# Kernel optimization log

Measured on AMD Instinct MI355X. Metric: run time of the kernel, lower is better.

The kernel has to match this reference:

```python
import jax, jax.numpy as jnp
import numpy as np

EPS = 1e-6

def setup_inputs() -> dict:
    key = jax.random.key(0)
    kq, kk, kv = jax.random.split(key, 3)
    B, H, S, D = 4, 16, 2048, 64
    q = jax.random.normal(kq, (B, H, S, D), dtype=jnp.float32)
    k = jax.random.normal(kk, (B, H, S, D), dtype=jnp.float32)
    v = jax.random.normal(kv, (B, H, S, D), dtype=jnp.float32)
    return {"q": q, "k": k, "v": v}

def reference(q, k, v):
    # ReBASED parallel attention: squared QK^T scores, causal mask, sum-normalized.
    scale = q.shape[-1] ** (-0.5)
    q = q * scale
    # attn: [B, H, S, S]
    attn = jnp.einsum('bhqd,bhkd->bhqk', q, k)
    attn = attn * attn  # squared scores
    S = q.shape[-2]
    causal = jnp.tril(jnp.ones((S, S), dtype=bool))
    attn = jnp.where(causal, attn, 0.0)
    o = jnp.einsum('bhqk,bhkd->bhqd', attn, v)
    z = attn.sum(-1, keepdims=True)
    return o / (z + EPS)
```

## Files before the change

kernel.cpp:

```cpp
#include <hip/hip_runtime.h>
#include <hip/hip_bf16.h>


#define SEQ 2048
#define HD  64
#define BQ  128
#define BK  64
#define LQ  72
#define LV  76

typedef __attribute__((ext_vector_type(8))) short bf16x8;
typedef __attribute__((ext_vector_type(4))) short bf16x4;
typedef __attribute__((ext_vector_type(4))) float f32x4;

__device__ inline unsigned packbf(float a, float b) {
    __hip_bfloat162 h = __float22bfloat162_rn(make_float2(a, b));
    union { __hip_bfloat162 h2; unsigned u; } cv; cv.h2 = h; return cv.u;
}

__global__ __launch_bounds__(256, 2)
void rebased_r3_kernel(const float* __restrict__ qg,
                       const float* __restrict__ kg,
                       const float* __restrict__ vg,
                       float* __restrict__ og) {
    __shared__ __align__(16) unsigned short Qs[BQ][LQ];
    __shared__ __align__(16) unsigned short Ks[2][BK][LQ];
    __shared__ __align__(16) unsigned short Vst[2][HD][LV];

    const int t    = threadIdx.x;
    const int lane = t & 63;
    const int w    = t >> 6;
    const int li   = lane & 15;
    const int qd   = lane >> 4;
    const int pj   = blockIdx.x;
    const int head = blockIdx.y;
    const size_t base = (size_t)head * SEQ * HD;

    #pragma unroll
    for (int seg = 0; seg < 2; ++seg) {
        const int qt = seg ? pj : (15 - pj);
        const int ktmax = 2 * qt + 1;

        float4 qreg[8], kreg[4], vreg[4];
        {
            const float4* qsrc = (const float4*)(qg + base + (size_t)qt * BQ * HD);
            #pragma unroll
            for (int l = 0; l < 8; ++l) qreg[l] = qsrc[t + l * 256];
            const float4* ksrc = (const float4*)(kg + base);
            const float4* vsrc = (const float4*)(vg + base);
            #pragma unroll
            for (int l = 0; l < 4; ++l) kreg[l] = ksrc[t + l * 256];
            const int d4g = t & 15, rp = t >> 4;
            #pragma unroll
            for (int p = 0; p < 2; ++p) {
                int r0 = p * 32 + rp * 2;
                vreg[2 * p]     = vsrc[r0 * 16 + d4g];
                vreg[2 * p + 1] = vsrc[(r0 + 1) * 16 + d4g];
            }
        }
        __syncthreads();

        #pragma unroll
        for (int l = 0; l < 8; ++l) {
            int f = t + l * 256, row = f >> 4, d4 = (f & 15) << 2;
            unsigned* dst = (unsigned*)&Qs[row][d4];
            dst[0] = packbf(qreg[l].x * 0.125f, qreg[l].y * 0.125f);
            dst[1] = packbf(qreg[l].z * 0.125f, qreg[l].w * 0.125f);
        }
        #pragma unroll
        for (int l = 0; l < 4; ++l) {
            int row = (t >> 4) + l * 16, d4 = (t & 15) << 2;
            unsigned* dst = (unsigned*)&Ks[0][row][d4];
            dst[0] = packbf(kreg[l].x, kreg[l].y);
            dst[1] = packbf(kreg[l].z, kreg[l].w);
        }
        {
            const int d4g = t & 15, rp = t >> 4;
            #pragma unroll
            for (int p = 0; p < 2; ++p) {
                int r0 = p * 32 + rp * 2;
                float a0[4] = {vreg[2*p].x, vreg[2*p].y, vreg[2*p].z, vreg[2*p].w};
                float a1[4] = {vreg[2*p+1].x, vreg[2*p+1].y, vreg[2*p+1].z, vreg[2*p+1].w};
                #pragma unroll
                for (int j = 0; j < 4; ++j)
                    *(unsigned*)&Vst[0][d4g * 4 + j][r0] = packbf(a0[j], a1[j]);
            }
        }
        __syncthreads();

        f32x4 oacc[2][4];
        float zpart[2] = {0.f, 0.f};
        #pragma unroll
        for (int mt = 0; mt < 2; ++mt)
            #pragma unroll
            for (int nd = 0; nd < 4; ++nd) oacc[mt][nd] = (f32x4){0.f, 0.f, 0.f, 0.f};

        for (int kt = 0; kt <= ktmax; ++kt) {
            const int cur = kt & 1;

            if (kt < ktmax) {
                const float4* ksrc = (const float4*)(kg + base + (size_t)(kt + 1) * BK * HD);
                const float4* vsrc = (const float4*)(vg + base + (size_t)(kt + 1) * BK * HD);
                #pragma unroll
                for (int l = 0; l < 4; ++l) kreg[l] = ksrc[t + l * 256];
                const int d4g = t & 15, rp = t >> 4;
                #pragma unroll
                for (int p = 0; p < 2; ++p) {
                    int r0 = p * 32 + rp * 2;
                    vreg[2 * p]     = vsrc[r0 * 16 + d4g];
                    vreg[2 * p + 1] = vsrc[(r0 + 1) * 16 + d4g];
                }
            }

            const int qrow_min = qt * BQ + w * 32;
            const bool active   = (kt * BK <= qrow_min + 31);
            const bool needmask = (kt * BK + 63 > qrow_min);

            if (active) {
                f32x4 stt[4][2];
                #pragma unroll
                for (int nk = 0; nk < 4; ++nk)
                    #pragma unroll
                    for (int mt = 0; mt < 2; ++mt) stt[nk][mt] = (f32x4){0.f,0.f,0.f,0.f};
                #pragma unroll
                for (int ks = 0; ks < 2; ++ks) {
                    const int kb = ks * 32 + qd * 8;
                    bf16x8 kf[4], qf[2];
                    #pragma unroll
                    for (int nk = 0; nk < 4; ++nk)
                        kf[nk] = *(const bf16x8*)&Ks[cur][nk * 16 + li][kb];
                    #pragma unroll
                    for (int mt = 0; mt < 2; ++mt)
                        qf[mt] = *(const bf16x8*)&Qs[w * 32 + mt * 16 + li][kb];
                    #pragma unroll
                    for (int nk = 0; nk < 4; ++nk)
                        #pragma unroll
                        for (int mt = 0; mt < 2; ++mt)
                            stt[nk][mt] = __builtin_amdgcn_mfma_f32_16x16x32_bf16(
                                kf[nk], qf[mt], stt[nk][mt], 0, 0, 0);
                }

                unsigned pk[4][2][2];
                #pragma unroll
                for (int nk = 0; nk < 4; ++nk) {
                    const int kcb = kt * BK + nk * 16 + qd * 4;
                    #pragma unroll
                    for (int mt = 0; mt < 2; ++mt) {
                        const int qrow = qrow_min + mt * 16 + li;
                        float p[4];
                        #pragma unroll
                        for (int r = 0; r < 4; ++r) {
                            float s = stt[nk][mt][r];
                            if (needmask && (kcb + r > qrow)) s = 0.f;
                            p[r] = s * s;
                        }
                        zpart[mt] += (p[0] + p[1]) + (p[2] + p[3]);
                        pk[nk][mt][0] = packbf(p[0], p[1]);
                        pk[nk][mt][1] = packbf(p[2], p[3]);
                    }
                }

                #pragma unroll
                for (int ks16 = 0; ks16 < 4; ++ks16) {
                    bf16x4 av[2];
                    #pragma unroll
                    for (int mt = 0; mt < 2; ++mt) {
                        union { unsigned u[2]; bf16x4 v; } cv;
                        cv.u[0] = pk[ks16][mt][0]; cv.u[1] = pk[ks16][mt][1];
                        av[mt] = cv.v;
                    }
                    #pragma unroll
                    for (int nd = 0; nd < 4; ++nd) {
                        bf16x4 vf = *(const bf16x4*)&Vst[cur][nd * 16 + li][ks16 * 16 + qd * 4];
                        #pragma unroll
                        for (int mt = 0; mt < 2; ++mt)
                            oacc[mt][nd] = __builtin_amdgcn_mfma_f32_16x16x16bf16_1k(
                                av[mt], vf, oacc[mt][nd], 0, 0, 0);
                    }
                }
            }

            if (kt < ktmax) {
                const int nb = cur ^ 1;
                #pragma unroll
                for (int l = 0; l < 4; ++l) {
                    int row = (t >> 4) + l * 16, d4 = (t & 15) << 2;
                    unsigned* dst = (unsigned*)&Ks[nb][row][d4];
                    dst[0] = packbf(kreg[l].x, kreg[l].y);
                    dst[1] = packbf(kreg[l].z, kreg[l].w);
                }
                const int d4g = t & 15, rp = t >> 4;
                #pragma unroll
                for (int p = 0; p < 2; ++p) {
                    int r0 = p * 32 + rp * 2;
                    float a0[4] = {vreg[2*p].x, vreg[2*p].y, vreg[2*p].z, vreg[2*p].w};
                    float a1[4] = {vreg[2*p+1].x, vreg[2*p+1].y, vreg[2*p+1].z, vreg[2*p+1].w};
                    #pragma unroll
                    for (int j = 0; j < 4; ++j)
                        *(unsigned*)&Vst[nb][d4g * 4 + j][r0] = packbf(a0[j], a1[j]);
                }
            }
            __syncthreads();
        }

        float* odst = og + base + (size_t)qt * BQ * HD;
        #pragma unroll
        for (int mt = 0; mt < 2; ++mt) {
            float zf = zpart[mt];
            zf += __shfl_xor(zf, 16, 64);
            zf += __shfl_xor(zf, 32, 64);
            #pragma unroll
            for (int r = 0; r < 4; ++r) {
                float zr = __shfl(zf, qd * 4 + r, 64);
                float inv = 1.f / (zr + 1e-6f);
                int row = w * 32 + mt * 16 + qd * 4 + r;
                #pragma unroll
                for (int nd = 0; nd < 4; ++nd)
                    odst[row * HD + nd * 16 + li] = oacc[mt][nd][r] * inv;
            }
        }
    }
}

extern "C" void kernel_launch(void* const* d_in, const int* in_sizes, int n_in,
                              void* d_out, int out_size, void* d_ws, size_t ws_size,
                              hipStream_t stream) {
    const float* q = (const float*)d_in[0];
    const float* k = (const float*)d_in[1];
    const float* v = (const float*)d_in[2];
    float* out = (float*)d_out;

    dim3 grid(8, 64);
    dim3 block(256);
    rebased_r3_kernel<<<grid, block, 0, stream>>>(q, k, v, out);
}
```

Before: 209.3 us.

## Switch to 32x32x16 MFMA with Q fragments held in registers

Replaces the 16x16 MFMA tiles with 32x32x16 bf16 MFMA for both the QK^T and PV products. Each wave now loads its own Q rows straight from global memory into register fragments, so the shared Q tile and its LDS reads go away. The squared-score fragments are rearranged across half-waves with a shuffle to form the PV operand, and V is now stored in a padded row layout. This is meant to cut LDS traffic and MFMA instruction count. In exchange it adds cross-lane shuffles, a larger accumulator register footprint, and a transposed output store pattern.

```diff
diff --git a/kernel.cpp b/kernel.cpp
--- a/kernel.cpp
+++ b/kernel.cpp
@@ -6,51 +6,63 @@
 #define HD  64
 #define BQ  128
 #define BK  64
-#define LQ  72
-#define LV  76
-
-typedef __attribute__((ext_vector_type(8))) short bf16x8;
-typedef __attribute__((ext_vector_type(4))) short bf16x4;
-typedef __attribute__((ext_vector_type(4))) float f32x4;
+#define LK  72
+
+typedef __attribute__((ext_vector_type(8)))  short bf16x8;
+typedef __attribute__((ext_vector_type(16))) float f32x16;
 
 __device__ inline unsigned packbf(float a, float b) {
-    __hip_bfloat162 h = __float22bfloat162_rn(make_float2(a, b));
-    union { __hip_bfloat162 h2; unsigned u; } cv; cv.h2 = h; return cv.u;
+    __hip_bfloat162 hh = __float22bfloat162_rn(make_float2(a, b));
+    union { __hip_bfloat162 h2; unsigned u; } cv; cv.h2 = hh; return cv.u;
 }
 
 __global__ __launch_bounds__(256, 2)
-void rebased_r3_kernel(const float* __restrict__ qg,
+void rebased_r4_kernel(const float* __restrict__ qg,
                        const float* __restrict__ kg,
                        const float* __restrict__ vg,
                        float* __restrict__ og) {
-    __shared__ __align__(16) unsigned short Qs[BQ][LQ];
-    __shared__ __align__(16) unsigned short Ks[2][BK][LQ];
-    __shared__ __align__(16) unsigned short Vst[2][HD][LV];
+    __shared__ __align__(16) unsigned short Ks[2][BK][LK];
+    __shared__ __align__(16) unsigned short Vs[2][HD][LK];
 
     const int t    = threadIdx.x;
     const int lane = t & 63;
     const int w    = t >> 6;
-    const int li   = lane & 15;
-    const int qd   = lane >> 4;
+    const int l5   = lane & 31;
+    const int h    = lane >> 5;
     const int pj   = blockIdx.x;
     const int head = blockIdx.y;
     const size_t base = (size_t)head * SEQ * HD;
+    const int d4g = t & 15, rp = t >> 4;
 
     #pragma unroll
     for (int seg = 0; seg < 2; ++seg) {
         const int qt = seg ? pj : (15 - pj);
         const int ktmax = 2 * qt + 1;
-
-        float4 qreg[8], kreg[4], vreg[4];
+        const int qrow_min = qt * BQ + w * 32;
+        const int qrow = qrow_min + l5;
+
+        bf16x8 qf[4];
         {
-            const float4* qsrc = (const float4*)(qg + base + (size_t)qt * BQ * HD);
-            #pragma unroll
-            for (int l = 0; l < 8; ++l) qreg[l] = qsrc[t + l * 256];
+            const float* qp = qg + base + (size_t)qrow * HD + 8 * h;
+            #pragma unroll
+            for (int ds = 0; ds < 4; ++ds) {
+                float4 a = *(const float4*)(qp + ds * 16);
+                float4 b = *(const float4*)(qp + ds * 16 + 4);
+                union { unsigned u[4]; bf16x8 v; } cv;
+                cv.u[0] = packbf(a.x * 0.125f, a.y * 0.125f);
+                cv.u[1] = packbf(a.z * 0.125f, a.w * 0.125f);
+                cv.u[2] = packbf(b.x * 0.125f, b.y * 0.125f);
+                cv.u[3] = packbf(b.z * 0.125f, b.w * 0.125f);
+                qf[ds] = cv.v;
+            }
+        }
+
+        float4 kreg[4], vreg[4];
+        {
             const float4* ksrc = (const float4*)(kg + base);
             const float4* vsrc = (const float4*)(vg + base);
             #pragma unroll
             for (int l = 0; l < 4; ++l) kreg[l] = ksrc[t + l * 256];
-            const int d4g = t & 15, rp = t >> 4;
             #pragma unroll
             for (int p = 0; p < 2; ++p) {
                 int r0 = p * 32 + rp * 2;
@@ -61,39 +73,27 @@
         __syncthreads();
 
         #pragma unroll
-        for (int l = 0; l < 8; ++l) {
+        for (int l = 0; l < 4; ++l) {
             int f = t + l * 256, row = f >> 4, d4 = (f & 15) << 2;
-            unsigned* dst = (unsigned*)&Qs[row][d4];
-            dst[0] = packbf(qreg[l].x * 0.125f, qreg[l].y * 0.125f);
-            dst[1] = packbf(qreg[l].z * 0.125f, qreg[l].w * 0.125f);
-        }
-        #pragma unroll
-        for (int l = 0; l < 4; ++l) {
-            int row = (t >> 4) + l * 16, d4 = (t & 15) << 2;
             unsigned* dst = (unsigned*)&Ks[0][row][d4];
             dst[0] = packbf(kreg[l].x, kreg[l].y);
             dst[1] = packbf(kreg[l].z, kreg[l].w);
         }
-        {
-            const int d4g = t & 15, rp = t >> 4;
-            #pragma unroll
-            for (int p = 0; p < 2; ++p) {
-                int r0 = p * 32 + rp * 2;
-                float a0[4] = {vreg[2*p].x, vreg[2*p].y, vreg[2*p].z, vreg[2*p].w};
-                float a1[4] = {vreg[2*p+1].x, vreg[2*p+1].y, vreg[2*p+1].z, vreg[2*p+1].w};
-                #pragma unroll
-                for (int j = 0; j < 4; ++j)
-                    *(unsigned*)&Vst[0][d4g * 4 + j][r0] = packbf(a0[j], a1[j]);
-            }
+        #pragma unroll
+        for (int p = 0; p < 2; ++p) {
+            int r0 = p * 32 + rp * 2;
+            float a0[4] = {vreg[2*p].x, vreg[2*p].y, vreg[2*p].z, vreg[2*p].w};
+            float a1[4] = {vreg[2*p+1].x, vreg[2*p+1].y, vreg[2*p+1].z, vreg[2*p+1].w};
+            #pragma unroll
+            for (int j = 0; j < 4; ++j)
+                *(unsigned*)&Vs[0][d4g * 4 + j][r0] = packbf(a0[j], a1[j]);
         }
         __syncthreads();
 
-        f32x4 oacc[2][4];
-        float zpart[2] = {0.f, 0.f};
-        #pragma unroll
-        for (int mt = 0; mt < 2; ++mt)
-            #pragma unroll
-            for (int nd = 0; nd < 4; ++nd) oacc[mt][nd] = (f32x4){0.f, 0.f, 0.f, 0.f};
+        f32x16 oa0, oa1;
+        #pragma unroll
+        for (int i = 0; i < 16; ++i) { oa0[i] = 0.f; oa1[i] = 0.f; }
+        float zadd = 0.f;
 
         for (int kt = 0; kt <= ktmax; ++kt) {
             const int cur = kt & 1;
@@ -103,7 +103,6 @@
                 const float4* vsrc = (const float4*)(vg + base + (size_t)(kt + 1) * BK * HD);
                 #pragma unroll
                 for (int l = 0; l < 4; ++l) kreg[l] = ksrc[t + l * 256];
-                const int d4g = t & 15, rp = t >> 4;
                 #pragma unroll
                 for (int p = 0; p < 2; ++p) {
                     int r0 = p * 32 + rp * 2;
@@ -112,71 +111,56 @@
                 }
             }
 
-            const int qrow_min = qt * BQ + w * 32;
-            const bool active   = (kt * BK <= qrow_min + 31);
-            const bool needmask = (kt * BK + 63 > qrow_min);
-
-            if (active) {
-                f32x4 stt[4][2];
-                #pragma unroll
-                for (int nk = 0; nk < 4; ++nk)
+            if (kt * 64 <= qrow_min + 31) {
+                f32x16 st0, st1;
+                #pragma unroll
+                for (int i = 0; i < 16; ++i) { st0[i] = 0.f; st1[i] = 0.f; }
+                #pragma unroll
+                for (int ds = 0; ds < 4; ++ds) {
+                    bf16x8 k0 = *(const bf16x8*)&Ks[cur][l5][ds * 16 + 8 * h];
+                    bf16x8 k1 = *(const bf16x8*)&Ks[cur][32 + l5][ds * 16 + 8 * h];
+                    st0 = __builtin_amdgcn_mfma_f32_32x32x16_bf16(k0, qf[ds], st0, 0, 0, 0);
+                    st1 = __builtin_amdgcn_mfma_f32_32x32x16_bf16(k1, qf[ds], st1, 0, 0, 0);
+                }
+
+                unsigned ppk[2][4][2];
+                const bool needmask = (kt * 64 + 63 > qrow_min);
+                const int kbase = kt * 64 + 4 * h;
+                #pragma unroll
+                for (int Mt = 0; Mt < 2; ++Mt) {
                     #pragma unroll
-                    for (int mt = 0; mt < 2; ++mt) stt[nk][mt] = (f32x4){0.f,0.f,0.f,0.f};
-                #pragma unroll
-                for (int ks = 0; ks < 2; ++ks) {
-                    const int kb = ks * 32 + qd * 8;
-                    bf16x8 kf[4], qf[2];
-                    #pragma unroll
-                    for (int nk = 0; nk < 4; ++nk)
-                        kf[nk] = *(const bf16x8*)&Ks[cur][nk * 16 + li][kb];
-                    #pragma unroll
-                    for (int mt = 0; mt < 2; ++mt)
-                        qf[mt] = *(const bf16x8*)&Qs[w * 32 + mt * 16 + li][kb];
-                    #pragma unroll
-                    for (int nk = 0; nk < 4; ++nk)
-                        #pragma unroll
-                        for (int mt = 0; mt < 2; ++mt)
-                            stt[nk][mt] = __builtin_amdgcn_mfma_f32_16x16x32_bf16(
-                                kf[nk], qf[mt], stt[nk][mt], 0, 0, 0);
-                }
-
-                unsigned pk[4][2][2];
-                #pragma unroll
-                for (int nk = 0; nk < 4; ++nk) {
-                    const int kcb = kt * BK + nk * 16 + qd * 4;
-                    #pragma unroll
-                    for (int mt = 0; mt < 2; ++mt) {
-                        const int qrow = qrow_min + mt * 16 + li;
+                    for (int r2 = 0; r2 < 4; ++r2) {
                         float p[4];
                         #pragma unroll
-                        for (int r = 0; r < 4; ++r) {
-                            float s = stt[nk][mt][r];
-                            if (needmask && (kcb + r > qrow)) s = 0.f;
-                            p[r] = s * s;
+                        for (int e = 0; e < 4; ++e) {
+                            float s = Mt ? st1[4 * r2 + e] : st0[4 * r2 + e];
+                            float pv = s * s;
+                            if (needmask && (kbase + 32 * Mt + 8 * r2 + e > qrow)) pv = 0.f;
+                            p[e] = pv;
                         }
-                        zpart[mt] += (p[0] + p[1]) + (p[2] + p[3]);
-                        pk[nk][mt][0] = packbf(p[0], p[1]);
-                        pk[nk][mt][1] = packbf(p[2], p[3]);
+                        zadd += (p[0] + p[1]) + (p[2] + p[3]);
+                        ppk[Mt][r2][0] = packbf(p[0], p[1]);
+                        ppk[Mt][r2][1] = packbf(p[2], p[3]);
                     }
                 }
 
                 #pragma unroll
-                for (int ks16 = 0; ks16 < 4; ++ks16) {
-                    bf16x4 av[2];
-                    #pragma unroll
-                    for (int mt = 0; mt < 2; ++mt) {
-                        union { unsigned u[2]; bf16x4 v; } cv;
-                        cv.u[0] = pk[ks16][mt][0]; cv.u[1] = pk[ks16][mt][1];
-                        av[mt] = cv.v;
-                    }
-                    #pragma unroll
-                    for (int nd = 0; nd < 4; ++nd) {
-                        bf16x4 vf = *(const bf16x4*)&Vst[cur][nd * 16 + li][ks16 * 16 + qd * 4];
-                        #pragma unroll
-                        for (int mt = 0; mt < 2; ++mt)
-                            oacc[mt][nd] = __builtin_amdgcn_mfma_f32_16x16x16bf16_1k(
-                                av[mt], vf, oacc[mt][nd], 0, 0, 0);
-                    }
+                for (int kst = 0; kst < 4; ++kst) {
+                    const int b0 = 2 * kst, b1 = 2 * kst + 1;
+                    unsigned a0 = ppk[b0 >> 2][b0 & 3][0], a1 = ppk[b0 >> 2][b0 & 3][1];
+                    unsigned c0 = ppk[b1 >> 2][b1 & 3][0], c1 = ppk[b1 >> 2][b1 & 3][1];
+                    unsigned s0 = h ? a0 : c0, s1 = h ? a1 : c1;
+                    unsigned g0 = (unsigned)__shfl_xor((int)s0, 32, 64);
+                    unsigned g1 = (unsigned)__shfl_xor((int)s1, 32, 64);
+                    union { unsigned u[4]; bf16x8 v; } pa;
+                    pa.u[0] = h ? g0 : a0;
+                    pa.u[1] = h ? g1 : a1;
+                    pa.u[2] = h ? c0 : g0;
+                    pa.u[3] = h ? c1 : g1;
+                    bf16x8 v0 = *(const bf16x8*)&Vs[cur][l5][kst * 16 + 8 * h];
+                    bf16x8 v1 = *(const bf16x8*)&Vs[cur][32 + l5][kst * 16 + 8 * h];
+                    oa0 = __builtin_amdgcn_mfma_f32_32x32x16_bf16(pa.v, v0, oa0, 0, 0, 0);
+                    oa1 = __builtin_amdgcn_mfma_f32_32x32x16_bf16(pa.v, v1, oa1, 0, 0, 0);
                 }
             }
 
@@ -184,12 +168,11 @@
                 const int nb = cur ^ 1;
                 #pragma unroll
                 for (int l = 0; l < 4; ++l) {
-                    int row = (t >> 4) + l * 16, d4 = (t & 15) << 2;
+                    int f = t + l * 256, row = f >> 4, d4 = (f & 15) << 2;
                     unsigned* dst = (unsigned*)&Ks[nb][row][d4];
                     dst[0] = packbf(kreg[l].x, kreg[l].y);
                     dst[1] = packbf(kreg[l].z, kreg[l].w);
                 }
-                const int d4g = t & 15, rp = t >> 4;
                 #pragma unroll
                 for (int p = 0; p < 2; ++p) {
                     int r0 = p * 32 + rp * 2;
@@ -197,27 +180,22 @@
                     float a1[4] = {vreg[2*p+1].x, vreg[2*p+1].y, vreg[2*p+1].z, vreg[2*p+1].w};
                     #pragma unroll
                     for (int j = 0; j < 4; ++j)
-                        *(unsigned*)&Vst[nb][d4g * 4 + j][r0] = packbf(a0[j], a1[j]);
+                        *(unsigned*)&Vs[nb][d4g * 4 + j][r0] = packbf(a0[j], a1[j]);
                 }
             }
             __syncthreads();
         }
 
-        float* odst = og + base + (size_t)qt * BQ * HD;
-        #pragma unroll
-        for (int mt = 0; mt < 2; ++mt) {
-            float zf = zpart[mt];
-            zf += __shfl_xor(zf, 16, 64);
-            zf += __shfl_xor(zf, 32, 64);
-            #pragma unroll
-            for (int r = 0; r < 4; ++r) {
-                float zr = __shfl(zf, qd * 4 + r, 64);
-                float inv = 1.f / (zr + 1e-6f);
-                int row = w * 32 + mt * 16 + qd * 4 + r;
-                #pragma unroll
-                for (int nd = 0; nd < 4; ++nd)
-                    odst[row * HD + nd * 16 + li] = oacc[mt][nd][r] * inv;
-            }
+        float zf = zadd + __shfl_xor(zadd, 32, 64);
+        float zinv = 1.f / (zf + 1e-6f);
+        float* odst = og + base + (size_t)(qt * BQ) * HD;
+        #pragma unroll
+        for (int r = 0; r < 16; ++r) {
+            int rowi = (r & 3) + 8 * (r >> 2) + 4 * h;
+            float inv = __shfl(zinv, rowi, 64);
+            int rg = w * 32 + rowi;
+            odst[(size_t)rg * HD + l5]      = oa0[r] * inv;
+            odst[(size_t)rg * HD + 32 + l5] = oa1[r] * inv;
         }
     }
 }
@@ -232,5 +210,5 @@
 
     dim3 grid(8, 64);
     dim3 block(256);
-    rebased_r3_kernel<<<grid, block, 0, stream>>>(q, k, v, out);
+    rebased_r4_kernel<<<grid, block, 0, stream>>>(q, k, v, out);
 }
```

Result: no change. 211.2 us (+0.9%).

## Shrink query tile to 64 rows with register-resident Q and remapped 1D grid

Applied to the files above, without the earlier changes.

Cuts the query tile from 128 to 64 rows, so each wave handles 16 query rows. Q fragments are loaded straight from global memory into registers, and the Q shared-memory buffer is removed. The grid becomes 1D with 1024 blocks in a head-interleaved order, and launch bounds are raised to 4 blocks per SM. This targets higher occupancy and finer causal load balance. In exchange, K/V tiles are loaded and converted twice as often per query row, and the wave-level skip of inactive key tiles is dropped.

```diff
diff --git a/kernel.cpp b/kernel.cpp
--- a/kernel.cpp
+++ b/kernel.cpp
@@ -4,9 +4,8 @@
 
 #define SEQ 2048
 #define HD  64
-#define BQ  128
 #define BK  64
-#define LQ  72
+#define LK  72
 #define LV  76
 
 typedef __attribute__((ext_vector_type(8))) short bf16x8;
@@ -14,17 +13,16 @@
 typedef __attribute__((ext_vector_type(4))) float f32x4;
 
 __device__ inline unsigned packbf(float a, float b) {
-    __hip_bfloat162 h = __float22bfloat162_rn(make_float2(a, b));
-    union { __hip_bfloat162 h2; unsigned u; } cv; cv.h2 = h; return cv.u;
+    __hip_bfloat162 hh = __float22bfloat162_rn(make_float2(a, b));
+    union { __hip_bfloat162 h2; unsigned u; } cv; cv.h2 = hh; return cv.u;
 }
 
-__global__ __launch_bounds__(256, 2)
-void rebased_r3_kernel(const float* __restrict__ qg,
+__global__ __launch_bounds__(256, 4)
+void rebased_r5_kernel(const float* __restrict__ qg,
                        const float* __restrict__ kg,
                        const float* __restrict__ vg,
                        float* __restrict__ og) {
-    __shared__ __align__(16) unsigned short Qs[BQ][LQ];
-    __shared__ __align__(16) unsigned short Ks[2][BK][LQ];
+    __shared__ __align__(16) unsigned short Ks[2][BK][LK];
     __shared__ __align__(16) unsigned short Vst[2][HD][LV];
 
     const int t    = threadIdx.x;
@@ -32,25 +30,42 @@
     const int w    = t >> 6;
     const int li   = lane & 15;
     const int qd   = lane >> 4;
-    const int pj   = blockIdx.x;
-    const int head = blockIdx.y;
+    const int id   = blockIdx.x;
+    const int xm   = id & 7;
+    const int qq   = id >> 3;
+    const int pj   = qq & 15;
+    const int head = xm + 8 * (qq >> 4);
     const size_t base = (size_t)head * SEQ * HD;
+    const int d4g = t & 15, rp = t >> 4;
 
     #pragma unroll
     for (int seg = 0; seg < 2; ++seg) {
-        const int qt = seg ? pj : (15 - pj);
-        const int ktmax = 2 * qt + 1;
-
-        float4 qreg[8], kreg[4], vreg[4];
+        const int qt = seg ? pj : (31 - pj);
+        const int ktmax = qt;
+        const int qrow = qt * 64 + w * 16 + li;
+
+        bf16x8 qf[2];
         {
-            const float4* qsrc = (const float4*)(qg + base + (size_t)qt * BQ * HD);
-            #pragma unroll
-            for (int l = 0; l < 8; ++l) qreg[l] = qsrc[t + l * 256];
+            const float* qp = qg + base + (size_t)qrow * HD + qd * 8;
+            #pragma unroll
+            for (int ks = 0; ks < 2; ++ks) {
+                float4 a = *(const float4*)(qp + ks * 32);
+                float4 b = *(const float4*)(qp + ks * 32 + 4);
+                union { unsigned u[4]; bf16x8 v; } cv;
+                cv.u[0] = packbf(a.x * 0.125f, a.y * 0.125f);
+                cv.u[1] = packbf(a.z * 0.125f, a.w * 0.125f);
+                cv.u[2] = packbf(b.x * 0.125f, b.y * 0.125f);
+                cv.u[3] = packbf(b.z * 0.125f, b.w * 0.125f);
+                qf[ks] = cv.v;
+            }
+        }
+
+        float4 kreg[4], vreg[4];
+        {
             const float4* ksrc = (const float4*)(kg + base);
             const float4* vsrc = (const float4*)(vg + base);
             #pragma unroll
             for (int l = 0; l < 4; ++l) kreg[l] = ksrc[t + l * 256];
-            const int d4g = t & 15, rp = t >> 4;
             #pragma unroll
             for (int p = 0; p < 2; ++p) {
                 int r0 = p * 32 + rp * 2;
@@ -61,39 +76,27 @@
         __syncthreads();
 
         #pragma unroll
-        for (int l = 0; l < 8; ++l) {
+        for (int l = 0; l < 4; ++l) {
             int f = t + l * 256, row = f >> 4, d4 = (f & 15) << 2;
-            unsigned* dst = (unsigned*)&Qs[row][d4];
-            dst[0] = packbf(qreg[l].x * 0.125f, qreg[l].y * 0.125f);
-            dst[1] = packbf(qreg[l].z * 0.125f, qreg[l].w * 0.125f);
-        }
-        #pragma unroll
-        for (int l = 0; l < 4; ++l) {
-            int row = (t >> 4) + l * 16, d4 = (t & 15) << 2;
             unsigned* dst = (unsigned*)&Ks[0][row][d4];
             dst[0] = packbf(kreg[l].x, kreg[l].y);
             dst[1] = packbf(kreg[l].z, kreg[l].w);
         }
-        {
-            const int d4g = t & 15, rp = t >> 4;
-            #pragma unroll
-            for (int p = 0; p < 2; ++p) {
-                int r0 = p * 32 + rp * 2;
-                float a0[4] = {vreg[2*p].x, vreg[2*p].y, vreg[2*p].z, vreg[2*p].w};
-                float a1[4] = {vreg[2*p+1].x, vreg[2*p+1].y, vreg[2*p+1].z, vreg[2*p+1].w};
-                #pragma unroll
-                for (int j = 0; j < 4; ++j)
-                    *(unsigned*)&Vst[0][d4g * 4 + j][r0] = packbf(a0[j], a1[j]);
-            }
+        #pragma unroll
+        for (int p = 0; p < 2; ++p) {
+            int r0 = p * 32 + rp * 2;
+            float a0[4] = {vreg[2*p].x, vreg[2*p].y, vreg[2*p].z, vreg[2*p].w};
+            float a1[4] = {vreg[2*p+1].x, vreg[2*p+1].y, vreg[2*p+1].z, vreg[2*p+1].w};
+            #pragma unroll
+            for (int j = 0; j < 4; ++j)
+                *(unsigned*)&Vst[0][d4g * 4 + j][r0] = packbf(a0[j], a1[j]);
         }
         __syncthreads();
 
-        f32x4 oacc[2][4];
-        float zpart[2] = {0.f, 0.f};
-        #pragma unroll
-        for (int mt = 0; mt < 2; ++mt)
-            #pragma unroll
-            for (int nd = 0; nd < 4; ++nd) oacc[mt][nd] = (f32x4){0.f, 0.f, 0.f, 0.f};
+        f32x4 oacc[4];
+        #pragma unroll
+        for (int nd = 0; nd < 4; ++nd) oacc[nd] = (f32x4){0.f, 0.f, 0.f, 0.f};
+        float zpart = 0.f;
 
         for (int kt = 0; kt <= ktmax; ++kt) {
             const int cur = kt & 1;
@@ -103,7 +106,6 @@
                 const float4* vsrc = (const float4*)(vg + base + (size_t)(kt + 1) * BK * HD);
                 #pragma unroll
                 for (int l = 0; l < 4; ++l) kreg[l] = ksrc[t + l * 256];
-                const int d4g = t & 15, rp = t >> 4;
                 #pragma unroll
                 for (int p = 0; p < 2; ++p) {
                     int r0 = p * 32 + rp * 2;
@@ -112,71 +114,49 @@
                 }
             }
 
-            const int qrow_min = qt * BQ + w * 32;
-            const bool active   = (kt * BK <= qrow_min + 31);
-            const bool needmask = (kt * BK + 63 > qrow_min);
-
-            if (active) {
-                f32x4 stt[4][2];
+            f32x4 stt[4];
+            #pragma unroll
+            for (int nk = 0; nk < 4; ++nk) stt[nk] = (f32x4){0.f, 0.f, 0.f, 0.f};
+            #pragma unroll
+            for (int ks = 0; ks < 2; ++ks) {
+                const int kb = ks * 32 + qd * 8;
+                bf16x8 kf[4];
                 #pragma unroll
                 for (int nk = 0; nk < 4; ++nk)
-                    #pragma unroll
-                    for (int mt = 0; mt < 2; ++mt) stt[nk][mt] = (f32x4){0.f,0.f,0.f,0.f};
-                #pragma unroll
-                for (int ks = 0; ks < 2; ++ks) {
-                    const int kb = ks * 32 + qd * 8;
-                    bf16x8 kf[4], qf[2];
-                    #pragma unroll
-                    for (int nk = 0; nk < 4; ++nk)
-                        kf[nk] = *(const bf16x8*)&Ks[cur][nk * 16 + li][kb];
-                    #pragma unroll
-                    for (int mt = 0; mt < 2; ++mt)
-                        qf[mt] = *(const bf16x8*)&Qs[w * 32 + mt * 16 + li][kb];
-                    #pragma unroll
-                    for (int nk = 0; nk < 4; ++nk)
-                        #pragma unroll
-                        for (int mt = 0; mt < 2; ++mt)
-                            stt[nk][mt] = __builtin_amdgcn_mfma_f32_16x16x32_bf16(
-                                kf[nk], qf[mt], stt[nk][mt], 0, 0, 0);
-                }
-
-                unsigned pk[4][2][2];
-                #pragma unroll
-                for (int nk = 0; nk < 4; ++nk) {
-                    const int kcb = kt * BK + nk * 16 + qd * 4;
-                    #pragma unroll
-                    for (int mt = 0; mt < 2; ++mt) {
-                        const int qrow = qrow_min + mt * 16 + li;
-                        float p[4];
-                        #pragma unroll
-                        for (int r = 0; r < 4; ++r) {
-                            float s = stt[nk][mt][r];
-                            if (needmask && (kcb + r > qrow)) s = 0.f;
-                            p[r] = s * s;
-                        }
-                        zpart[mt] += (p[0] + p[1]) + (p[2] + p[3]);
-                        pk[nk][mt][0] = packbf(p[0], p[1]);
-                        pk[nk][mt][1] = packbf(p[2], p[3]);
-                    }
-                }
-
-                #pragma unroll
-                for (int ks16 = 0; ks16 < 4; ++ks16) {
-                    bf16x4 av[2];
-                    #pragma unroll
-                    for (int mt = 0; mt < 2; ++mt) {
-                        union { unsigned u[2]; bf16x4 v; } cv;
-                        cv.u[0] = pk[ks16][mt][0]; cv.u[1] = pk[ks16][mt][1];
-                        av[mt] = cv.v;
-                    }
-                    #pragma unroll
-                    for (int nd = 0; nd < 4; ++nd) {
-                        bf16x4 vf = *(const bf16x4*)&Vst[cur][nd * 16 + li][ks16 * 16 + qd * 4];
-                        #pragma unroll
-                        for (int mt = 0; mt < 2; ++mt)
-                            oacc[mt][nd] = __builtin_amdgcn_mfma_f32_16x16x16bf16_1k(
-                                av[mt], vf, oacc[mt][nd], 0, 0, 0);
-                    }
+                    kf[nk] = *(const bf16x8*)&Ks[cur][nk * 16 + li][kb];
+                #pragma unroll
+                for (int nk = 0; nk < 4; ++nk)
+                    stt[nk] = __builtin_amdgcn_mfma_f32_16x16x32_bf16(
+                        kf[nk], qf[ks], stt[nk], 0, 0, 0);
+            }
+
+            unsigned pk[4][2];
+            const bool needmask = (kt == qt);
+            #pragma unroll
+            for (int nk = 0; nk < 4; ++nk) {
+                const int kcb = kt * 64 + nk * 16 + qd * 4;
+                float p[4];
+                #pragma unroll
+                for (int r = 0; r < 4; ++r) {
+                    float s = stt[nk][r];
+                    float pv = s * s;
+                    if (needmask && (kcb + r > qrow)) pv = 0.f;
+                    p[r] = pv;
+                }
+                zpart += (p[0] + p[1]) + (p[2] + p[3]);
+                pk[nk][0] = packbf(p[0], p[1]);
+                pk[nk][1] = packbf(p[2], p[3]);
+            }
+
+            #pragma unroll
+            for (int ks16 = 0; ks16 < 4; ++ks16) {
+                union { unsigned u[2]; bf16x4 v; } av;
+                av.u[0] = pk[ks16][0]; av.u[1] = pk[ks16][1];
+                #pragma unroll
+                for (int nd = 0; nd < 4; ++nd) {
+                    bf16x4 vf = *(const bf16x4*)&Vst[cur][nd * 16 + li][ks16 * 16 + qd * 4];
+                    oacc[nd] = __builtin_amdgcn_mfma_f32_16x16x16bf16_1k(
+                        av.v, vf, oacc[nd], 0, 0, 0);
                 }
             }
 
@@ -184,12 +164,11 @@
                 const int nb = cur ^ 1;
                 #pragma unroll
                 for (int l = 0; l < 4; ++l) {
-                    int row = (t >> 4) + l * 16, d4 = (t & 15) << 2;
+                    int f = t + l * 256, row = f >> 4, d4 = (f & 15) << 2;
                     unsigned* dst = (unsigned*)&Ks[nb][row][d4];
                     dst[0] = packbf(kreg[l].x, kreg[l].y);
                     dst[1] = packbf(kreg[l].z, kreg[l].w);
                 }
-                const int d4g = t & 15, rp = t >> 4;
                 #pragma unroll
                 for (int p = 0; p < 2; ++p) {
                     int r0 = p * 32 + rp * 2;
@@ -203,21 +182,18 @@
             __syncthreads();
         }
 
-        float* odst = og + base + (size_t)qt * BQ * HD;
-        #pragma unroll
-        for (int mt = 0; mt < 2; ++mt) {
-            float zf = zpart[mt];
-            zf += __shfl_xor(zf, 16, 64);
-            zf += __shfl_xor(zf, 32, 64);
-            #pragma unroll
-            for (int r = 0; r < 4; ++r) {
-                float zr = __shfl(zf, qd * 4 + r, 64);
-                float inv = 1.f / (zr + 1e-6f);
-                int row = w * 32 + mt * 16 + qd * 4 + r;
-                #pragma unroll
-                for (int nd = 0; nd < 4; ++nd)
-                    odst[row * HD + nd * 16 + li] = oacc[mt][nd][r] * inv;
-            }
+        float zf = zpart;
+        zf += __shfl_xor(zf, 16, 64);
+        zf += __shfl_xor(zf, 32, 64);
+        float zinv = 1.f / (zf + 1e-6f);
+        float* odst = og + base + (size_t)(qt * 64) * HD;
+        #pragma unroll
+        for (int r = 0; r < 4; ++r) {
+            float inv = __shfl(zinv, qd * 4 + r, 64);
+            int rowl = w * 16 + qd * 4 + r;
+            #pragma unroll
+            for (int nd = 0; nd < 4; ++nd)
+                odst[(size_t)rowl * HD + nd * 16 + li] = oacc[nd][r] * inv;
         }
     }
 }
@@ -230,7 +206,7 @@
     const float* v = (const float*)d_in[2];
     float* out = (float*)d_out;
 
-    dim3 grid(8, 64);
+    dim3 grid(1024);
     dim3 block(256);
-    rebased_r3_kernel<<<grid, block, 0, stream>>>(q, k, v, out);
+    rebased_r5_kernel<<<grid, block, 0, stream>>>(q, k, v, out);
 }
```

Result: slower. 228.3 us (+9.1%).
